# Kernel optimization log

Hardware: AMD Instinct MI355X
Metric: run time of the kernel (lower is better)

## Reference

```python
import jax, jax.numpy as jnp
import numpy as np

B, IN, G, F = 8192, 1024, 100, 128  # batch, input_size, n_models, n_feature per group
L = [100, 100, 50]                   # tree_layers
BN_EPS = 1e-5


def batch_dense(h, w, b):
    # h: [B, G, I], w: [G, I, O], b: [G, O] -> [B, G, O]
    return jnp.einsum('bgi,gio->bgo', h, w) + b


def batch_norm(h, gamma, beta):
    # training-mode BatchNorm1d over batch dim; h: [B, F]
    mu = jnp.mean(h, axis=0)
    var = jnp.var(h, axis=0)  # biased variance, matching torch BN normalization
    return (h - mu) * jax.lax.rsqrt(var + BN_EPS) * gamma + beta


def setup_inputs() -> dict:
    key = jax.random.key(0)
    ks = jax.random.split(key, 16)
    x = jax.random.normal(ks[0], (B, IN), dtype=jnp.float32)
    used_features = jax.random.randint(ks[1], (G * F,), 0, IN, dtype=jnp.int32)
    s = 0.05
    w0 = jax.random.normal(ks[2], (G, F, L[0]), dtype=jnp.float32) * s
    b0 = jax.random.normal(ks[3], (G, L[0]), dtype=jnp.float32) * s
    w1 = jax.random.normal(ks[4], (G, L[0], L[1]), dtype=jnp.float32) * s
    b1 = jax.random.normal(ks[5], (G, L[1]), dtype=jnp.float32) * s
    w2 = jax.random.normal(ks[6], (G, L[1], L[2]), dtype=jnp.float32) * s
    b2 = jax.random.normal(ks[7], (G, L[2]), dtype=jnp.float32) * s
    gamma0 = jnp.ones((G * L[0],), dtype=jnp.float32)
    beta0 = jnp.zeros((G * L[0],), dtype=jnp.float32)
    gamma1 = jnp.ones((G * L[1],), dtype=jnp.float32)
    beta1 = jnp.zeros((G * L[1],), dtype=jnp.float32)
    out_weight = jax.random.normal(ks[8], (G * L[2], 1), dtype=jnp.float32) * s
    out_bias = jax.random.normal(ks[9], (1,), dtype=jnp.float32) * s
    return {'x': x, 'used_features': used_features,
            'w0': w0, 'b0': b0, 'w1': w1, 'b1': b1, 'w2': w2, 'b2': b2,
            'gamma0': gamma0, 'beta0': beta0, 'gamma1': gamma1, 'beta1': beta1,
            'out_weight': out_weight, 'out_bias': out_bias}


def reference(x, used_features, w0, b0, w1, b1, w2, b2,
              gamma0, beta0, gamma1, beta1, out_weight, out_bias):
    bsz = x.shape[0]
    g = w0.shape[0]
    # gather selected features, split into per-model groups
    h = jnp.take(x, used_features, axis=1).reshape(bsz, g, -1)  # [B, G, F]
    # layer 0: per-group dense -> BN -> ReLU
    h = batch_dense(h, w0, b0).reshape(bsz, -1)
    h = jax.nn.relu(batch_norm(h, gamma0, beta0)).reshape(bsz, g, -1)
    # layer 1
    h = batch_dense(h, w1, b1).reshape(bsz, -1)
    h = jax.nn.relu(batch_norm(h, gamma1, beta1)).reshape(bsz, g, -1)
    # final per-group dense -> tree embedding prediction
    pred = batch_dense(h, w2, b2).reshape(bsz, -1)  # [B, G*L[-1]]
    out = out_bias + pred @ out_weight              # addmm, [B, 1]
    return jax.nn.sigmoid(out), pred
```

## Files before the change

kernel.cpp:

```cpp
#include <hip/hip_runtime.h>

#define B_SZ 8192
#define IN_SZ 1024
#define G_SZ 100
#define F_SZ 128

using f32x4 = __attribute__((ext_vector_type(4))) float;
using s16x8 = __attribute__((ext_vector_type(8))) short;
typedef __bf16 bf16x8 __attribute__((ext_vector_type(8)));

__device__ __forceinline__ short cvt_bf16(float f) {
    __bf16 h = (__bf16)f;
    return __builtin_bit_cast(short, h);
}
__device__ __forceinline__ float bfs2f(short s) {
    union { unsigned u; float f; } v; v.u = ((unsigned)(unsigned short)s) << 16;
    return v.f;
}

__global__ __launch_bounds__(256) void k_gather(const float* __restrict__ x,
                                                const int* __restrict__ uf,
                                                unsigned short* __restrict__ Ag) {
    __shared__ __align__(16) unsigned short xrow[16][1032];
    const int t = threadIdx.x;
    const int b0 = blockIdx.x * 16;
    #pragma unroll
    for (int i = 0; i < 16; ++i) {
        int c4 = t + i * 256;
        int r = c4 >> 8;
        int cc = (c4 & 255) << 2;
        float4 v = *reinterpret_cast<const float4*>(&x[(size_t)(b0 + r) * IN_SZ + cc]);
        ushort4 o;
        o.x = (unsigned short)cvt_bf16(v.x); o.y = (unsigned short)cvt_bf16(v.y);
        o.z = (unsigned short)cvt_bf16(v.z); o.w = (unsigned short)cvt_bf16(v.w);
        *reinterpret_cast<ushort4*>(&xrow[r][cc]) = o;
    }
    __syncthreads();
    for (int i = 0; i < 200; ++i) {
        int c = t + i * 256;
        int ch = c & 31; int r = (c >> 5) & 15; int g = c >> 9;
        int4 id = *reinterpret_cast<const int4*>(&uf[g * F_SZ + ch * 4]);
        ushort4 o;
        o.x = xrow[r][id.x]; o.y = xrow[r][id.y]; o.z = xrow[r][id.z]; o.w = xrow[r][id.w];
        *reinterpret_cast<ushort4*>(&Ag[(((size_t)g * B_SZ + b0 + r) << 7) + ch * 4]) = o;
    }
}

template<int K_SRC, int N_OUT, int NT, bool FOLD>
__device__ __forceinline__ void pack_one(int e, const float* __restrict__ W,
                                         const float* __restrict__ bias,
                                         unsigned short* __restrict__ P) {
    constexpr int EPG = 4 * NT * 64;
    int g = e / EPG; int r = e - g * EPG;
    int lane = r & 63; int nt = (r >> 6) % NT; int ks = r / (64 * NT);
    int n = nt * 16 + (lane & 15); int kb = ks * 32 + (lane >> 4) * 8;
    s16x8 v;
    #pragma unroll
    for (int j = 0; j < 8; ++j) {
        int k = kb + j; float val = 0.f;
        if (n < N_OUT) {
            if (k < K_SRC) val = W[((size_t)g * K_SRC + k) * N_OUT + n];
            else if (FOLD && k == K_SRC) val = bias[g * N_OUT + n];
        }
        v[j] = cvt_bf16(val);
    }
    *reinterpret_cast<s16x8*>(&P[(size_t)e * 8]) = v;
}

__global__ __launch_bounds__(256) void k_packW(
    const float* __restrict__ w0,
    const float* __restrict__ w1, const float* __restrict__ b1,
    const float* __restrict__ w2, const float* __restrict__ b2,
    unsigned short* __restrict__ p0, unsigned short* __restrict__ p1,
    unsigned short* __restrict__ p2) {
    int id = blockIdx.x * 256 + threadIdx.x;
    if (id < 179200)       pack_one<128, 100, 7, false>(id, w0, nullptr, p0);
    else if (id < 358400)  pack_one<100, 100, 7, true >(id - 179200, w1, b1, p1);
    else                   pack_one<100,  50, 4, true >(id - 358400, w2, b2, p2);
}

template<int K_SRC, int N_OUT, int NT, bool BN_IN, bool IS_LAST, bool HAS_BIAS>
__global__ __launch_bounds__(256, 4) void k_dense(
    const unsigned short* __restrict__ Ain,
    const unsigned short* __restrict__ Wf,
    const float* __restrict__ bias,
    const float* __restrict__ sa, const float* __restrict__ sb,
    unsigned short* __restrict__ Hout,
    float* __restrict__ pred,
    float* __restrict__ ssum, float* __restrict__ ssq,
    const float* __restrict__ ow, float* __restrict__ out_acc)
{
    constexpr int EPG = 4 * NT * 64;
    __shared__ __align__(16) unsigned short LH[IS_LAST ? 16 : 128 * 104];
    __shared__ __align__(16) float LP[IS_LAST ? 128 * 52 : 16];
    __shared__ float ls1[IS_LAST ? 1 : NT * 16];
    __shared__ float ls2[IS_LAST ? 1 : NT * 16];

    const int t = threadIdx.x;
    const int g = blockIdx.x >> 6;
    const int m0 = (blockIdx.x & 63) << 7;
    const int lane = t & 63, wid = t >> 6;
    const int lr = lane & 15, lg = lane >> 4;

    if constexpr (!IS_LAST) {
        if (t < NT * 16) { ls1[t] = 0.f; ls2[t] = 0.f; }
    }

    const unsigned short* wbase = Wf + ((size_t)g * EPG + lane) * 8;

    s16x8 a[2][4];
    if constexpr (K_SRC == 128) {
        const unsigned short* r0 = Ain + ((size_t)g * B_SZ + m0 + wid * 32 + lr) * 128;
        #pragma unroll
        for (int ks = 0; ks < 4; ++ks) {
            const int kb = ks * 32 + lg * 8;
            a[0][ks] = *reinterpret_cast<const s16x8*>(r0 + kb);
            a[1][ks] = *reinterpret_cast<const s16x8*>(r0 + 16 * 128 + kb);
        }
    } else {
        const unsigned short* r0 = Ain + ((size_t)g * B_SZ + m0 + wid * 32 + lr) * 100;
        #pragma unroll
        for (int ks = 0; ks < 3; ++ks) {
            const int kb = ks * 32 + lg * 8;
            #pragma unroll
            for (int h = 0; h < 2; ++h) {
                reinterpret_cast<short4*>(&a[h][ks])[0] =
                    *reinterpret_cast<const short4*>(r0 + h * 16 * 100 + kb);
                reinterpret_cast<short4*>(&a[h][ks])[1] =
                    *reinterpret_cast<const short4*>(r0 + h * 16 * 100 + kb + 4);
            }
        }
        a[0][3] = s16x8{}; a[1][3] = s16x8{};
        if (lg == 0) {
            reinterpret_cast<short4*>(&a[0][3])[0] =
                *reinterpret_cast<const short4*>(r0 + 96);
            reinterpret_cast<short4*>(&a[1][3])[0] =
                *reinterpret_cast<const short4*>(r0 + 16 * 100 + 96);
        }
    }

    #define APP(vv, idx, s, o) { float f_ = bfs2f(vv[idx]) * (s) + (o); \
                                 vv[idx] = cvt_bf16(fmaxf(f_, 0.f)); }
    if constexpr (BN_IN) {
        #pragma unroll
        for (int ks = 0; ks < 3; ++ks) {
            const int kb = ks * 32 + lg * 8;
            float4 S0 = *reinterpret_cast<const float4*>(&sa[g * 128 + kb]);
            float4 S1 = *reinterpret_cast<const float4*>(&sa[g * 128 + kb + 4]);
            float4 O0 = *reinterpret_cast<const float4*>(&sb[g * 128 + kb]);
            float4 O1 = *reinterpret_cast<const float4*>(&sb[g * 128 + kb + 4]);
            #pragma unroll
            for (int h = 0; h < 2; ++h) {
                APP(a[h][ks],0,S0.x,O0.x) APP(a[h][ks],1,S0.y,O0.y)
                APP(a[h][ks],2,S0.z,O0.z) APP(a[h][ks],3,S0.w,O0.w)
                APP(a[h][ks],4,S1.x,O1.x) APP(a[h][ks],5,S1.y,O1.y)
                APP(a[h][ks],6,S1.z,O1.z) APP(a[h][ks],7,S1.w,O1.w)
            }
        }
        if (lg == 0) {
            float4 S0 = *reinterpret_cast<const float4*>(&sa[g * 128 + 96]);
            float4 O0 = *reinterpret_cast<const float4*>(&sb[g * 128 + 96]);
            #pragma unroll
            for (int h = 0; h < 2; ++h) {
                APP(a[h][3],0,S0.x,O0.x) APP(a[h][3],1,S0.y,O0.y)
                APP(a[h][3],2,S0.z,O0.z) APP(a[h][3],3,S0.w,O0.w)
                a[h][3][4] = (short)0x3F80;
            }
        }
    }
    #undef APP

    f32x4 acc[2][NT] = {};
    #pragma unroll
    for (int ks = 0; ks < 4; ++ks) {
        bf16x8 av0 = __builtin_bit_cast(bf16x8, a[0][ks]);
        bf16x8 av1 = __builtin_bit_cast(bf16x8, a[1][ks]);
        #pragma unroll
        for (int nt = 0; nt < NT; ++nt) {
            s16x8 b = *reinterpret_cast<const s16x8*>(wbase + (size_t)((ks * NT + nt) * 64) * 8);
            bf16x8 bv = __builtin_bit_cast(bf16x8, b);
            if constexpr (IS_LAST) {
                acc[0][nt] = __builtin_amdgcn_mfma_f32_16x16x32_bf16(bv, av0, acc[0][nt], 0, 0, 0);
                acc[1][nt] = __builtin_amdgcn_mfma_f32_16x16x32_bf16(bv, av1, acc[1][nt], 0, 0, 0);
            } else {
                acc[0][nt] = __builtin_amdgcn_mfma_f32_16x16x32_bf16(av0, bv, acc[0][nt], 0, 0, 0);
                acc[1][nt] = __builtin_amdgcn_mfma_f32_16x16x32_bf16(av1, bv, acc[1][nt], 0, 0, 0);
            }
        }
    }

    if constexpr (!IS_LAST) {
        __syncthreads();
        #pragma unroll
        for (int nt = 0; nt < NT; ++nt) {
            const int col = nt * 16 + lr;
            const bool valid = col < N_OUT;
            float bv = 0.f;
            if constexpr (HAS_BIAS) bv = valid ? bias[g * N_OUT + col] : 0.f;
            float s1 = 0.f, s2 = 0.f;
            #pragma unroll
            for (int mi = 0; mi < 2; ++mi) {
                const int rloc = wid * 32 + mi * 16 + (lg << 2);
                #pragma unroll
                for (int r = 0; r < 4; ++r) {
                    float v = acc[mi][nt][r] + bv;
                    short hb = cvt_bf16(v);
                    float vq = bfs2f(hb);
                    s1 += vq; s2 += vq * vq;
                    if (valid) LH[(rloc + r) * 104 + col] = (unsigned short)hb;
                }
            }
            s1 += __shfl_xor(s1, 16); s1 += __shfl_xor(s1, 32);
            s2 += __shfl_xor(s2, 16); s2 += __shfl_xor(s2, 32);
            if (valid && lg == 0) {
                atomicAdd(&ls1[col], s1);
                atomicAdd(&ls2[col], s2);
            }
        }
        __syncthreads();
        if (t < N_OUT) {
            atomicAdd(&ssum[g * N_OUT + t], ls1[t]);
            atomicAdd(&ssq[g * N_OUT + t], ls2[t]);
        }
        #pragma unroll
        for (int i = 0; i < 13; ++i) {
            int e = t + i * 256;
            if (e < 3200) {
                int row = e / 25;
                int c4 = (e - row * 25) * 4;
                ushort4 v = *reinterpret_cast<const ushort4*>(&LH[row * 104 + c4]);
                *reinterpret_cast<ushort4*>(
                    Hout + ((size_t)g * B_SZ + m0 + row) * 100 + c4) = v;
            }
        }
    } else {
        #pragma unroll
        for (int mi = 0; mi < 2; ++mi) {
            const int bl = wid * 32 + mi * 16 + lr;
            float dp = 0.f;
            #pragma unroll
            for (int nt = 0; nt < NT; ++nt) {
                const int n0 = nt * 16 + (lg << 2);
                f32x4 v = acc[mi][nt];
                if (nt < 3) {
                    float2 w01 = *reinterpret_cast<const float2*>(&ow[g * N_OUT + n0]);
                    float2 w23 = *reinterpret_cast<const float2*>(&ow[g * N_OUT + n0 + 2]);
                    dp += v[0] * w01.x + v[1] * w01.y + v[2] * w23.x + v[3] * w23.y;
                    LP[bl * 52 + n0 + 0] = v[0]; LP[bl * 52 + n0 + 1] = v[1];
                    LP[bl * 52 + n0 + 2] = v[2]; LP[bl * 52 + n0 + 3] = v[3];
                } else if (lg == 0) {
                    float2 w01 = *reinterpret_cast<const float2*>(&ow[g * N_OUT + n0]);
                    dp += v[0] * w01.x + v[1] * w01.y;
                    LP[bl * 52 + n0 + 0] = v[0]; LP[bl * 52 + n0 + 1] = v[1];
                }
            }
            dp += __shfl_xor(dp, 16); dp += __shfl_xor(dp, 32);
            if (lg == 0) atomicAdd(&out_acc[m0 + bl], dp);
        }
        __syncthreads();
        #pragma unroll
        for (int i = 0; i < 13; ++i) {
            int e = t + i * 256;
            if (e < 3200) {
                int row = e / 25;
                int c2 = e - row * 25;
                float2 v = *reinterpret_cast<const float2*>(&LP[row * 52 + c2 * 2]);
                *reinterpret_cast<float2*>(
                    &pred[(size_t)(m0 + row) * 5000 + g * N_OUT + c2 * 2]) = v;
            }
        }
    }
}

__global__ __launch_bounds__(256) void k_bnfin(const float* __restrict__ ssum,
                                               const float* __restrict__ ssq,
                                               const float* __restrict__ gamma,
                                               const float* __restrict__ beta,
                                               float* __restrict__ sa,
                                               float* __restrict__ sb) {
    int c = blockIdx.x * 256 + threadIdx.x;
    if (c < G_SZ * 128) {
        int g = c >> 7, ch = c & 127;
        float s, o;
        if (ch < 100) {
            float mean = ssum[g * 100 + ch] * (1.f / 8192.f);
            float var = ssq[g * 100 + ch] * (1.f / 8192.f) - mean * mean;
            s = rsqrtf(var + 1e-5f) * gamma[g * 100 + ch];
            o = beta[g * 100 + ch] - mean * s;
        } else { s = 1.f; o = 0.f; }
        sa[c] = s; sb[c] = o;
    }
}

__global__ __launch_bounds__(256) void k_sig(const float* __restrict__ out_acc,
                                             const float* __restrict__ ob,
                                             float* __restrict__ out) {
    int b = blockIdx.x * 256 + threadIdx.x;
    if (b < B_SZ) {
        float v = ob[0] + out_acc[b];
        out[b] = 1.f / (1.f + expf(-v));
    }
}

extern "C" void kernel_launch(void* const* d_in, const int* in_sizes, int n_in,
                              void* d_out, int out_size, void* d_ws, size_t ws_size,
                              hipStream_t stream) {
    const float* x      = (const float*)d_in[0];
    const int*   uf     = (const int*)d_in[1];
    const float* w0     = (const float*)d_in[2];
    const float* b0     = (const float*)d_in[3];
    const float* w1     = (const float*)d_in[4];
    const float* b1     = (const float*)d_in[5];
    const float* w2     = (const float*)d_in[6];
    const float* b2     = (const float*)d_in[7];
    const float* gamma0 = (const float*)d_in[8];
    const float* beta0  = (const float*)d_in[9];
    const float* gamma1 = (const float*)d_in[10];
    const float* beta1  = (const float*)d_in[11];
    const float* ow     = (const float*)d_in[12];
    const float* ob     = (const float*)d_in[13];

    char* ws = (char*)d_ws;
    const size_t AG_BYTES = (size_t)G_SZ * B_SZ * 128 * 2;
    unsigned short* Ag = (unsigned short*)ws;
    unsigned short* h1 = Ag;
    float* stat = (float*)(ws + AG_BYTES);
    float* sum0    = stat;
    float* ssq0    = stat + 10000;
    float* sum1    = stat + 20000;
    float* ssq1    = stat + 30000;
    float* out_acc = stat + 40000;
    float* sa0     = stat + 48192;
    float* sb0     = stat + 60992;
    float* sa1     = stat + 73792;
    float* sb1     = stat + 86592;

    unsigned short* p0 = (unsigned short*)(ws + AG_BYTES + 397568);
    unsigned short* p1 = p0 + (size_t)179200 * 8;
    unsigned short* p2 = p1 + (size_t)179200 * 8;

    unsigned short* h0 = (unsigned short*)((float*)d_out + B_SZ);
    float* pred = (float*)d_out + B_SZ;
    float* sig  = (float*)d_out;

    hipMemsetAsync(stat, 0, 48192 * sizeof(float), stream);

    k_packW<<<1800, 256, 0, stream>>>(w0, w1, b1, w2, b2, p0, p1, p2);
    k_gather<<<B_SZ / 16, 256, 0, stream>>>(x, uf, Ag);

    k_dense<128, 100, 7, false, false, true><<<6400, 256, 0, stream>>>(
        Ag, p0, b0, nullptr, nullptr, h0, nullptr, sum0, ssq0, nullptr, nullptr);
    k_bnfin<<<50, 256, 0, stream>>>(sum0, ssq0, gamma0, beta0, sa0, sb0);

    k_dense<100, 100, 7, true, false, false><<<6400, 256, 0, stream>>>(
        h0, p1, nullptr, sa0, sb0, h1, nullptr, sum1, ssq1, nullptr, nullptr);
    k_bnfin<<<50, 256, 0, stream>>>(sum1, ssq1, gamma1, beta1, sa1, sb1);

    k_dense<100, 50, 4, true, true, false><<<6400, 256, 0, stream>>>(
        h1, p2, nullptr, sa1, sb1, nullptr, pred, nullptr, nullptr, ow, out_acc);

    k_sig<<<32, 256, 0, stream>>>(out_acc, ob, sig);
}
```

Measured before the change: 433.0 us.

## Process two batch tiles per block with software-pipelined A loads

Each dense block now handles two 128-row batch tiles instead of one, halving the grid. The second tile's activation loads are issued before the first tile's LDS store phase so they overlap. BN statistics are accumulated in registers across both tiles, so the LDS and global atomics run once per block, and the bias is loaded once. Lighter custom barriers replace __syncthreads. In exchange, register pressure rises from holding two A fragment sets, and there are fewer blocks to spread across the CUs.

```diff
diff --git a/kernel.cpp b/kernel.cpp
--- a/kernel.cpp
+++ b/kernel.cpp
@@ -16,6 +16,13 @@
 __device__ __forceinline__ float bfs2f(short s) {
     union { unsigned u; float f; } v; v.u = ((unsigned)(unsigned short)s) << 16;
     return v.f;
+}
+
+__device__ __forceinline__ void bar_lds() {
+    __builtin_amdgcn_sched_barrier(0);
+    asm volatile("s_waitcnt lgkmcnt(0)" ::: "memory");
+    __builtin_amdgcn_s_barrier();
+    __builtin_amdgcn_sched_barrier(0);
 }
 
 __global__ __launch_bounds__(256) void k_gather(const float* __restrict__ x,
@@ -97,8 +104,9 @@
     __shared__ float ls2[IS_LAST ? 1 : NT * 16];
 
     const int t = threadIdx.x;
-    const int g = blockIdx.x >> 6;
-    const int m0 = (blockIdx.x & 63) << 7;
+    const int g = blockIdx.x >> 5;
+    const int mt0 = (blockIdx.x & 31) << 1;
+    const int m0_0 = mt0 << 7, m0_1 = (mt0 + 1) << 7;
     const int lane = t & 63, wid = t >> 6;
     const int lr = lane & 15, lg = lane >> 4;
 
@@ -108,40 +116,52 @@
 
     const unsigned short* wbase = Wf + ((size_t)g * EPG + lane) * 8;
 
-    s16x8 a[2][4];
-    if constexpr (K_SRC == 128) {
-        const unsigned short* r0 = Ain + ((size_t)g * B_SZ + m0 + wid * 32 + lr) * 128;
-        #pragma unroll
-        for (int ks = 0; ks < 4; ++ks) {
-            const int kb = ks * 32 + lg * 8;
-            a[0][ks] = *reinterpret_cast<const s16x8*>(r0 + kb);
-            a[1][ks] = *reinterpret_cast<const s16x8*>(r0 + 16 * 128 + kb);
-        }
-    } else {
-        const unsigned short* r0 = Ain + ((size_t)g * B_SZ + m0 + wid * 32 + lr) * 100;
-        #pragma unroll
-        for (int ks = 0; ks < 3; ++ks) {
-            const int kb = ks * 32 + lg * 8;
-            #pragma unroll
-            for (int h = 0; h < 2; ++h) {
-                reinterpret_cast<short4*>(&a[h][ks])[0] =
-                    *reinterpret_cast<const short4*>(r0 + h * 16 * 100 + kb);
-                reinterpret_cast<short4*>(&a[h][ks])[1] =
-                    *reinterpret_cast<const short4*>(r0 + h * 16 * 100 + kb + 4);
-            }
-        }
-        a[0][3] = s16x8{}; a[1][3] = s16x8{};
-        if (lg == 0) {
-            reinterpret_cast<short4*>(&a[0][3])[0] =
-                *reinterpret_cast<const short4*>(r0 + 96);
-            reinterpret_cast<short4*>(&a[1][3])[0] =
-                *reinterpret_cast<const short4*>(r0 + 16 * 100 + 96);
-        }
-    }
+    float rs1[NT] = {}, rs2[NT] = {};
+    float bvn[NT];
+    #pragma unroll
+    for (int nt = 0; nt < NT; ++nt) {
+        bvn[nt] = 0.f;
+        if constexpr (HAS_BIAS) {
+            int col = nt * 16 + lr;
+            if (col < N_OUT) bvn[nt] = bias[g * N_OUT + col];
+        }
+    }
+
+    auto load_a = [&](s16x8 (&a)[2][4], int m0) {
+        if constexpr (K_SRC == 128) {
+            const unsigned short* r0 = Ain + ((size_t)g * B_SZ + m0 + wid * 32 + lr) * 128;
+            #pragma unroll
+            for (int ks = 0; ks < 4; ++ks) {
+                const int kb = ks * 32 + lg * 8;
+                a[0][ks] = *reinterpret_cast<const s16x8*>(r0 + kb);
+                a[1][ks] = *reinterpret_cast<const s16x8*>(r0 + 16 * 128 + kb);
+            }
+        } else {
+            const unsigned short* r0 = Ain + ((size_t)g * B_SZ + m0 + wid * 32 + lr) * 100;
+            #pragma unroll
+            for (int ks = 0; ks < 3; ++ks) {
+                const int kb = ks * 32 + lg * 8;
+                #pragma unroll
+                for (int h = 0; h < 2; ++h) {
+                    reinterpret_cast<short4*>(&a[h][ks])[0] =
+                        *reinterpret_cast<const short4*>(r0 + h * 16 * 100 + kb);
+                    reinterpret_cast<short4*>(&a[h][ks])[1] =
+                        *reinterpret_cast<const short4*>(r0 + h * 16 * 100 + kb + 4);
+                }
+            }
+            a[0][3] = s16x8{}; a[1][3] = s16x8{};
+            if (lg == 0) {
+                reinterpret_cast<short4*>(&a[0][3])[0] =
+                    *reinterpret_cast<const short4*>(r0 + 96);
+                reinterpret_cast<short4*>(&a[1][3])[0] =
+                    *reinterpret_cast<const short4*>(r0 + 16 * 100 + 96);
+            }
+        }
+    };
 
     #define APP(vv, idx, s, o) { float f_ = bfs2f(vv[idx]) * (s) + (o); \
                                  vv[idx] = cvt_bf16(fmaxf(f_, 0.f)); }
-    if constexpr (BN_IN) {
+    auto bn_a = [&](s16x8 (&a)[2][4]) {
         #pragma unroll
         for (int ks = 0; ks < 3; ++ks) {
             const int kb = ks * 32 + lg * 8;
@@ -167,61 +187,55 @@
                 a[h][3][4] = (short)0x3F80;
             }
         }
-    }
+    };
     #undef APP
 
-    f32x4 acc[2][NT] = {};
-    #pragma unroll
-    for (int ks = 0; ks < 4; ++ks) {
-        bf16x8 av0 = __builtin_bit_cast(bf16x8, a[0][ks]);
-        bf16x8 av1 = __builtin_bit_cast(bf16x8, a[1][ks]);
-        #pragma unroll
-        for (int nt = 0; nt < NT; ++nt) {
-            s16x8 b = *reinterpret_cast<const s16x8*>(wbase + (size_t)((ks * NT + nt) * 64) * 8);
-            bf16x8 bv = __builtin_bit_cast(bf16x8, b);
-            if constexpr (IS_LAST) {
-                acc[0][nt] = __builtin_amdgcn_mfma_f32_16x16x32_bf16(bv, av0, acc[0][nt], 0, 0, 0);
-                acc[1][nt] = __builtin_amdgcn_mfma_f32_16x16x32_bf16(bv, av1, acc[1][nt], 0, 0, 0);
-            } else {
-                acc[0][nt] = __builtin_amdgcn_mfma_f32_16x16x32_bf16(av0, bv, acc[0][nt], 0, 0, 0);
-                acc[1][nt] = __builtin_amdgcn_mfma_f32_16x16x32_bf16(av1, bv, acc[1][nt], 0, 0, 0);
-            }
-        }
-    }
-
-    if constexpr (!IS_LAST) {
-        __syncthreads();
+    f32x4 acc[2][NT];
+    auto mfma_a = [&](s16x8 (&a)[2][4]) {
+        #pragma unroll
+        for (int mi = 0; mi < 2; ++mi)
+            #pragma unroll
+            for (int nt = 0; nt < NT; ++nt)
+                acc[mi][nt] = f32x4{};
+        #pragma unroll
+        for (int ks = 0; ks < 4; ++ks) {
+            bf16x8 av0 = __builtin_bit_cast(bf16x8, a[0][ks]);
+            bf16x8 av1 = __builtin_bit_cast(bf16x8, a[1][ks]);
+            #pragma unroll
+            for (int nt = 0; nt < NT; ++nt) {
+                s16x8 b = *reinterpret_cast<const s16x8*>(wbase + (size_t)((ks * NT + nt) * 64) * 8);
+                bf16x8 bv = __builtin_bit_cast(bf16x8, b);
+                if constexpr (IS_LAST) {
+                    acc[0][nt] = __builtin_amdgcn_mfma_f32_16x16x32_bf16(bv, av0, acc[0][nt], 0, 0, 0);
+                    acc[1][nt] = __builtin_amdgcn_mfma_f32_16x16x32_bf16(bv, av1, acc[1][nt], 0, 0, 0);
+                } else {
+                    acc[0][nt] = __builtin_amdgcn_mfma_f32_16x16x32_bf16(av0, bv, acc[0][nt], 0, 0, 0);
+                    acc[1][nt] = __builtin_amdgcn_mfma_f32_16x16x32_bf16(av1, bv, acc[1][nt], 0, 0, 0);
+                }
+            }
+        }
+    };
+
+    auto lh_write = [&]() {
         #pragma unroll
         for (int nt = 0; nt < NT; ++nt) {
             const int col = nt * 16 + lr;
             const bool valid = col < N_OUT;
-            float bv = 0.f;
-            if constexpr (HAS_BIAS) bv = valid ? bias[g * N_OUT + col] : 0.f;
-            float s1 = 0.f, s2 = 0.f;
             #pragma unroll
             for (int mi = 0; mi < 2; ++mi) {
                 const int rloc = wid * 32 + mi * 16 + (lg << 2);
                 #pragma unroll
                 for (int r = 0; r < 4; ++r) {
-                    float v = acc[mi][nt][r] + bv;
+                    float v = acc[mi][nt][r] + bvn[nt];
                     short hb = cvt_bf16(v);
                     float vq = bfs2f(hb);
-                    s1 += vq; s2 += vq * vq;
+                    rs1[nt] += vq; rs2[nt] += vq * vq;
                     if (valid) LH[(rloc + r) * 104 + col] = (unsigned short)hb;
                 }
             }
-            s1 += __shfl_xor(s1, 16); s1 += __shfl_xor(s1, 32);
-            s2 += __shfl_xor(s2, 16); s2 += __shfl_xor(s2, 32);
-            if (valid && lg == 0) {
-                atomicAdd(&ls1[col], s1);
-                atomicAdd(&ls2[col], s2);
-            }
-        }
-        __syncthreads();
-        if (t < N_OUT) {
-            atomicAdd(&ssum[g * N_OUT + t], ls1[t]);
-            atomicAdd(&ssq[g * N_OUT + t], ls2[t]);
-        }
+        }
+    };
+    auto lh_store = [&](int m0) {
         #pragma unroll
         for (int i = 0; i < 13; ++i) {
             int e = t + i * 256;
@@ -233,7 +247,9 @@
                     Hout + ((size_t)g * B_SZ + m0 + row) * 100 + c4) = v;
             }
         }
-    } else {
+    };
+
+    auto lp_write_dot = [&](int m0) {
         #pragma unroll
         for (int mi = 0; mi < 2; ++mi) {
             const int bl = wid * 32 + mi * 16 + lr;
@@ -257,7 +273,8 @@
             dp += __shfl_xor(dp, 16); dp += __shfl_xor(dp, 32);
             if (lg == 0) atomicAdd(&out_acc[m0 + bl], dp);
         }
-        __syncthreads();
+    };
+    auto lp_store = [&](int m0) {
         #pragma unroll
         for (int i = 0; i < 13; ++i) {
             int e = t + i * 256;
@@ -269,6 +286,51 @@
                     &pred[(size_t)(m0 + row) * 5000 + g * N_OUT + c2 * 2]) = v;
             }
         }
+    };
+
+    s16x8 aA[2][4], aB[2][4];
+
+    load_a(aA, m0_0);
+    if constexpr (BN_IN) bn_a(aA);
+    mfma_a(aA);
+    if constexpr (!IS_LAST) {
+        lh_write();
+        load_a(aB, m0_1);
+        bar_lds();
+        lh_store(m0_0);
+        bar_lds();
+        if constexpr (BN_IN) bn_a(aB);
+        mfma_a(aB);
+        lh_write();
+        bar_lds();
+        lh_store(m0_1);
+        #pragma unroll
+        for (int nt = 0; nt < NT; ++nt) {
+            float s1 = rs1[nt], s2 = rs2[nt];
+            s1 += __shfl_xor(s1, 16); s1 += __shfl_xor(s1, 32);
+            s2 += __shfl_xor(s2, 16); s2 += __shfl_xor(s2, 32);
+            const int col = nt * 16 + lr;
+            if (col < N_OUT && lg == 0) {
+                atomicAdd(&ls1[col], s1);
+                atomicAdd(&ls2[col], s2);
+            }
+        }
+        bar_lds();
+        if (t < N_OUT) {
+            atomicAdd(&ssum[g * N_OUT + t], ls1[t]);
+            atomicAdd(&ssq[g * N_OUT + t], ls2[t]);
+        }
+    } else {
+        lp_write_dot(m0_0);
+        load_a(aB, m0_1);
+        bar_lds();
+        lp_store(m0_0);
+        bar_lds();
+        if constexpr (BN_IN) bn_a(aB);
+        mfma_a(aB);
+        lp_write_dot(m0_1);
+        bar_lds();
+        lp_store(m0_1);
     }
 }
 
@@ -348,15 +410,15 @@
     k_packW<<<1800, 256, 0, stream>>>(w0, w1, b1, w2, b2, p0, p1, p2);
     k_gather<<<B_SZ / 16, 256, 0, stream>>>(x, uf, Ag);
 
-    k_dense<128, 100, 7, false, false, true><<<6400, 256, 0, stream>>>(
+    k_dense<128, 100, 7, false, false, true><<<3200, 256, 0, stream>>>(
         Ag, p0, b0, nullptr, nullptr, h0, nullptr, sum0, ssq0, nullptr, nullptr);
     k_bnfin<<<50, 256, 0, stream>>>(sum0, ssq0, gamma0, beta0, sa0, sb0);
 
-    k_dense<100, 100, 7, true, false, false><<<6400, 256, 0, stream>>>(
+    k_dense<100, 100, 7, true, false, false><<<3200, 256, 0, stream>>>(
         h0, p1, nullptr, sa0, sb0, h1, nullptr, sum1, ssq1, nullptr, nullptr);
     k_bnfin<<<50, 256, 0, stream>>>(sum1, ssq1, gamma1, beta1, sa1, sb1);
 
-    k_dense<100, 50, 4, true, true, false><<<6400, 256, 0, stream>>>(
+    k_dense<100, 50, 4, true, true, false><<<3200, 256, 0, stream>>>(
         h1, p2, nullptr, sa1, sb1, nullptr, pred, nullptr, nullptr, ow, out_acc);
 
     k_sig<<<32, 256, 0, stream>>>(out_acc, ob, sig);
```

Measured after the change: 766.8 us. +77.1%, slower.

## Stage activation tiles via global_load_lds with XOR-swizzled gather layout

Applied to the files above, without the earlier changes.

The dense kernels now copy their 128-row activation tile straight from global memory into LDS with the direct global-to-LDS load, then read the MFMA A fragments out of LDS instead of doing per-lane strided global loads. The gather kernel writes its output with an XOR swizzle of 16-byte chunks keyed on the row, so the LDS reads for the K=128 layer avoid bank conflicts. The LDS tile shares a buffer with the epilogue bounce buffer, which needs an extra barrier before reuse. This adds a block-wide sync before compute and more LDS per block, which may reduce occupancy.

```diff
diff --git a/kernel.cpp b/kernel.cpp
--- a/kernel.cpp
+++ b/kernel.cpp
@@ -17,6 +17,10 @@
     union { unsigned u; float f; } v; v.u = ((unsigned)(unsigned short)s) << 16;
     return v.f;
 }
+
+#define GLDS(gp, lp) __builtin_amdgcn_global_load_lds( \
+    (const __attribute__((address_space(1))) void*)(gp), \
+    (__attribute__((address_space(3))) void*)(lp), 16, 0, 0)
 
 __global__ __launch_bounds__(256) void k_gather(const float* __restrict__ x,
                                                 const int* __restrict__ uf,
@@ -42,7 +46,9 @@
         int4 id = *reinterpret_cast<const int4*>(&uf[g * F_SZ + ch * 4]);
         ushort4 o;
         o.x = xrow[r][id.x]; o.y = xrow[r][id.y]; o.z = xrow[r][id.z]; o.w = xrow[r][id.w];
-        *reinterpret_cast<ushort4*>(&Ag[(((size_t)g * B_SZ + b0 + r) << 7) + ch * 4]) = o;
+        const int b = b0 + r;
+        const int di = ((((ch >> 1) ^ (b & 7)) << 3) | ((ch & 1) << 2));
+        *reinterpret_cast<ushort4*>(&Ag[(((size_t)g * B_SZ + b) << 7) + di]) = o;
     }
 }
 
@@ -91,8 +97,10 @@
     const float* __restrict__ ow, float* __restrict__ out_acc)
 {
     constexpr int EPG = 4 * NT * 64;
-    __shared__ __align__(16) unsigned short LH[IS_LAST ? 16 : 128 * 104];
-    __shared__ __align__(16) float LP[IS_LAST ? 128 * 52 : 16];
+    constexpr int TILE_BYTES = 128 * K_SRC * 2;
+    constexpr int BOUNCE = IS_LAST ? 128 * 52 * 4 : 128 * 104 * 2;
+    constexpr int UBYTES = TILE_BYTES > BOUNCE ? TILE_BYTES : BOUNCE;
+    __shared__ __align__(16) unsigned char U[UBYTES];
     __shared__ float ls1[IS_LAST ? 1 : NT * 16];
     __shared__ float ls2[IS_LAST ? 1 : NT * 16];
 
@@ -106,36 +114,51 @@
         if (t < NT * 16) { ls1[t] = 0.f; ls2[t] = 0.f; }
     }
 
+    constexpr int NI = TILE_BYTES / 1024;
+    const char* sbp = (const char*)(Ain + ((size_t)g * B_SZ + m0) * K_SRC);
+    #pragma unroll
+    for (int ji = 0; ji < (NI + 3) / 4; ++ji) {
+        int i = ji * 4 + wid;
+        if (i < NI) GLDS(sbp + i * 1024 + lane * 16, U + i * 1024);
+    }
+    __syncthreads();
+
     const unsigned short* wbase = Wf + ((size_t)g * EPG + lane) * 8;
 
     s16x8 a[2][4];
-    if constexpr (K_SRC == 128) {
-        const unsigned short* r0 = Ain + ((size_t)g * B_SZ + m0 + wid * 32 + lr) * 128;
-        #pragma unroll
-        for (int ks = 0; ks < 4; ++ks) {
-            const int kb = ks * 32 + lg * 8;
-            a[0][ks] = *reinterpret_cast<const s16x8*>(r0 + kb);
-            a[1][ks] = *reinterpret_cast<const s16x8*>(r0 + 16 * 128 + kb);
-        }
-    } else {
-        const unsigned short* r0 = Ain + ((size_t)g * B_SZ + m0 + wid * 32 + lr) * 100;
-        #pragma unroll
-        for (int ks = 0; ks < 3; ++ks) {
-            const int kb = ks * 32 + lg * 8;
-            #pragma unroll
-            for (int h = 0; h < 2; ++h) {
-                reinterpret_cast<short4*>(&a[h][ks])[0] =
-                    *reinterpret_cast<const short4*>(r0 + h * 16 * 100 + kb);
-                reinterpret_cast<short4*>(&a[h][ks])[1] =
-                    *reinterpret_cast<const short4*>(r0 + h * 16 * 100 + kb + 4);
-            }
-        }
-        a[0][3] = s16x8{}; a[1][3] = s16x8{};
-        if (lg == 0) {
-            reinterpret_cast<short4*>(&a[0][3])[0] =
-                *reinterpret_cast<const short4*>(r0 + 96);
-            reinterpret_cast<short4*>(&a[1][3])[0] =
-                *reinterpret_cast<const short4*>(r0 + 16 * 100 + 96);
+    {
+        const unsigned char* asb = U;
+        const int row0 = wid * 32 + lr, row1 = row0 + 16;
+        if constexpr (K_SRC == 128) {
+            #pragma unroll
+            for (int ks = 0; ks < 4; ++ks) {
+                const int c16 = ks * 4 + lg;
+                a[0][ks] = *reinterpret_cast<const s16x8*>(
+                    asb + row0 * 256 + ((c16 ^ (row0 & 7)) << 4));
+                a[1][ks] = *reinterpret_cast<const s16x8*>(
+                    asb + row1 * 256 + ((c16 ^ (row1 & 7)) << 4));
+            }
+        } else {
+            const int rb0 = row0 * 200, rb1 = row1 * 200;
+            #pragma unroll
+            for (int ks = 0; ks < 3; ++ks) {
+                const int kb2 = (ks * 32 + lg * 8) * 2;
+                reinterpret_cast<short4*>(&a[0][ks])[0] =
+                    *reinterpret_cast<const short4*>(asb + rb0 + kb2);
+                reinterpret_cast<short4*>(&a[0][ks])[1] =
+                    *reinterpret_cast<const short4*>(asb + rb0 + kb2 + 8);
+                reinterpret_cast<short4*>(&a[1][ks])[0] =
+                    *reinterpret_cast<const short4*>(asb + rb1 + kb2);
+                reinterpret_cast<short4*>(&a[1][ks])[1] =
+                    *reinterpret_cast<const short4*>(asb + rb1 + kb2 + 8);
+            }
+            a[0][3] = s16x8{}; a[1][3] = s16x8{};
+            if (lg == 0) {
+                reinterpret_cast<short4*>(&a[0][3])[0] =
+                    *reinterpret_cast<const short4*>(asb + rb0 + 192);
+                reinterpret_cast<short4*>(&a[1][3])[0] =
+                    *reinterpret_cast<const short4*>(asb + rb1 + 192);
+            }
         }
     }
 
@@ -190,6 +213,7 @@
     }
 
     if constexpr (!IS_LAST) {
+        unsigned short* LH = (unsigned short*)U;
         __syncthreads();
         #pragma unroll
         for (int nt = 0; nt < NT; ++nt) {
@@ -234,6 +258,8 @@
             }
         }
     } else {
+        float* LP = (float*)U;
+        __syncthreads();
         #pragma unroll
         for (int mi = 0; mi < 2; ++mi) {
             const int bl = wid * 32 + mi * 16 + lr;
```

After: 448.7 us. 3.6% more time.
